# Kernel tuning notes

Measured on AMD Instinct MI355X. Metric: run time of the kernel, lower is better.

## Reference

```python
import jax, jax.numpy as jnp
import numpy as np

B, N = 128, 128
FEAT_IN = 6   # feature_dim(4) + class + score
E = 32        # embedding_dim
NUM_CLASSES = 80


def setup_inputs() -> dict:
    key = jax.random.key(0)
    ks = jax.random.split(key, 20)
    def glorot(k, shape):
        fan_in, fan_out = shape[0], shape[1]
        lim = jnp.sqrt(6.0 / (fan_in + fan_out)).astype(jnp.float32)
        return jax.random.uniform(k, shape, jnp.float32, -lim, lim)
    return {
        'boxes': jax.random.uniform(ks[0], (B, N, 4), jnp.float32),
        'classes': jax.random.randint(ks[1], (B, N), 0, NUM_CLASSES),
        'scores': jax.random.uniform(ks[2], (B, N), jnp.float32),
        'num_objects': jax.random.randint(ks[3], (B,), 1, N + 1),
        # feature_encoder: Linear(6->32), ReLU, Linear(32->32)
        'W1': glorot(ks[4], (FEAT_IN, E)), 'b1': jnp.zeros((E,), jnp.float32),
        'W2': glorot(ks[5], (E, E)),       'b2': jnp.zeros((E,), jnp.float32),
        # isObject: Linear(32->32), ReLU, Linear(32->1), Sigmoid
        'Wo1': glorot(ks[6], (E, E)),  'bo1': jnp.zeros((E,), jnp.float32),
        'Wo2': glorot(ks[7], (E, 1)),  'bo2': jnp.zeros((1,), jnp.float32),
        # sameClass: Linear(64->32), ReLU, Linear(32->1), Sigmoid
        'Ws1': glorot(ks[8], (2 * E, E)), 'bs1': jnp.zeros((E,), jnp.float32),
        'Ws2': glorot(ks[9], (E, 1)),     'bs2': jnp.zeros((1,), jnp.float32),
    }


def reference(boxes, classes, scores, num_objects, W1, b1, W2, b2,
              Wo1, bo1, Wo2, bo2, Ws1, bs1, Ws2, bs2):
    # encode: [B,N,6] -> [B,N,E]
    combined = jnp.concatenate(
        [boxes, classes.astype(jnp.float32)[..., None], scores[..., None]], axis=-1)
    enc = jax.nn.relu(combined @ W1 + b1) @ W2 + b2                 # [B,N,E]

    # isObject predicate -> [B,N]
    isobj = jax.nn.sigmoid(jax.nn.relu(enc @ Wo1 + bo1) @ Wo2 + bo2)[..., 0]

    # sameClass on all pairs: split concat-weight so we never build [B,N,N,2E]
    Wsx, Wsy = Ws1[:E], Ws1[E:]
    hx = enc @ Wsx                                                  # [B,N,E]
    hy = enc @ Wsy                                                  # [B,N,E]
    h = jax.nn.relu(hx[:, :, None, :] + hy[:, None, :, :] + bs1)    # [B,N,N,E]
    same = jax.nn.sigmoid(h @ Ws2 + bs2)[..., 0]                    # [B,N,N] (x,y)

    # inner = And_min(isObject(y), sameClass(x,y))
    inner = jnp.minimum(isobj[:, None, :], same)                    # [B,N,N]

    mask = jnp.arange(N)[None, :] < num_objects[:, None]            # [B,N] valid objs
    n = num_objects.astype(jnp.float32)
    denom = jnp.maximum(n, 1.0)

    # Exists_y = mean over valid y
    exists = jnp.sum(inner * mask[:, None, :], axis=-1) / denom[:, None]  # [B,N]

    # outer = Or_max(Not(isObject(x)), exists)
    outer = jnp.maximum(1.0 - isobj, exists)                        # [B,N]

    # Forall_x = min over valid x (pad with 1.0, never the min for valid batches)
    sat_b = jnp.min(jnp.where(mask, outer, 1.0), axis=-1)           # [B]

    valid = (num_objects > 0).astype(jnp.float32)
    cnt = jnp.sum(valid)
    total = jnp.where(cnt > 0,
                      jnp.sum(sat_b * valid) / jnp.maximum(cnt, 1.0),
                      jnp.float32(1.0))
    return total
```

## Files before the change

### kernel.cpp

```cpp
#include <hip/hip_runtime.h>

#define BB 128
#define NN 128
#define EE 32


__global__ __launch_bounds__(512) void ltn_fused(
    const float* __restrict__ boxes, const int* __restrict__ classes,
    const float* __restrict__ scores, const int* __restrict__ num_objects,
    const float* __restrict__ W1, const float* __restrict__ b1,
    const float* __restrict__ W2, const float* __restrict__ b2,
    const float* __restrict__ Wo1, const float* __restrict__ bo1,
    const float* __restrict__ Wo2, const float* __restrict__ bo2,
    const float* __restrict__ Ws1, const float* __restrict__ bs1,
    const float* __restrict__ Ws2, const float* __restrict__ bs2,
    float* __restrict__ ws)
{
    __shared__ float hyS[128 * 36];
    __shared__ float hxS[64 * 36];
    __shared__ float rows[32 * 36];
    __shared__ float isoS[128];
    __shared__ float wred[8];

    const int t = threadIdx.x;
    const int b = blockIdx.x >> 1;
    const int half = blockIdx.x & 1;
    const int e = t & 31;
    const int g = t >> 5;

    const int nb = num_objects[b];

    float w1c[6];
#pragma unroll
    for (int f = 0; f < 6; f++) w1c[f] = W1[f * 32 + e];
    float w2c[32], wo1c[32], wsxc[32], wsyc[32];
#pragma unroll
    for (int k = 0; k < 32; k++) {
        w2c[k]  = W2[k * 32 + e];
        wo1c[k] = Wo1[k * 32 + e];
        wsxc[k] = Ws1[k * 32 + e];
        wsyc[k] = Ws1[(32 + k) * 32 + e];
    }
    const float b1e  = b1[e];
    const float b2e  = b2[e];
    const float bo1e = bo1[e];
    const float wo2e = Wo2[e];
    const float bo2s = bo2[0];

    const int il0 = g * 8;
#pragma unroll 2
    for (int it = 0; it < 8; ++it) {
        const int il = il0 + it;
        const int item = b * 128 + il;
        float* row = rows + (g * 2 + (it & 1)) * 36;

        const float4 bx = ((const float4*)boxes)[item];
        const float c4 = (float)classes[item];
        const float c5 = scores[item];

        float h1 = b1e;
        h1 = fmaf(bx.x, w1c[0], h1);
        h1 = fmaf(bx.y, w1c[1], h1);
        h1 = fmaf(bx.z, w1c[2], h1);
        h1 = fmaf(bx.w, w1c[3], h1);
        h1 = fmaf(c4,   w1c[4], h1);
        h1 = fmaf(c5,   w1c[5], h1);
        h1 = fmaxf(h1, 0.f);

        row[e] = h1;

        float a0 = 0.f, a1 = 0.f, a2 = 0.f, a3 = 0.f;
#pragma unroll
        for (int kk = 0; kk < 8; kk++) {
            const float4 h = *(const float4*)(row + kk * 4);
            a0 = fmaf(h.x, w2c[4 * kk + 0], a0);
            a1 = fmaf(h.y, w2c[4 * kk + 1], a1);
            a2 = fmaf(h.z, w2c[4 * kk + 2], a2);
            a3 = fmaf(h.w, w2c[4 * kk + 3], a3);
        }
        const float enc = ((a0 + a1) + (a2 + a3)) + b2e;
        row[e] = enc;

        float u = bo1e, hx = 0.f, hy = 0.f;
#pragma unroll
        for (int kk = 0; kk < 8; kk++) {
            const float4 ec = *(const float4*)(row + kk * 4);
            const int k0 = 4 * kk;
            u  = fmaf(ec.x, wo1c[k0 + 0], u);
            u  = fmaf(ec.y, wo1c[k0 + 1], u);
            u  = fmaf(ec.z, wo1c[k0 + 2], u);
            u  = fmaf(ec.w, wo1c[k0 + 3], u);
            hx = fmaf(ec.x, wsxc[k0 + 0], hx);
            hx = fmaf(ec.y, wsxc[k0 + 1], hx);
            hx = fmaf(ec.z, wsxc[k0 + 2], hx);
            hx = fmaf(ec.w, wsxc[k0 + 3], hx);
            hy = fmaf(ec.x, wsyc[k0 + 0], hy);
            hy = fmaf(ec.y, wsyc[k0 + 1], hy);
            hy = fmaf(ec.z, wsyc[k0 + 2], hy);
            hy = fmaf(ec.w, wsyc[k0 + 3], hy);
        }
        u = fmaxf(u, 0.f);

        float v = u * wo2e;
        v += __shfl_xor(v, 16, 32);
        v += __shfl_xor(v, 8, 32);
        v += __shfl_xor(v, 4, 32);
        v += __shfl_xor(v, 2, 32);
        v += __shfl_xor(v, 1, 32);

        hyS[il * 36 + e] = hy;
        if ((il >> 6) == half) hxS[(il & 63) * 36 + e] = hx;
        if (e == 0)
            isoS[il] = 1.f / (1.f + __expf(-(v + bo2s)));
    }
    __syncthreads();

    const int p  = t >> 4;
    const int li0 = half * 64 + 2 * p;
    const int li1 = li0 + 1;
    const int s  = t & 15;

    float hxb0[32], hxb1[32];
#pragma unroll
    for (int kk = 0; kk < 8; kk++) {
        const float4 a = ((const float4*)(hxS + (2 * p) * 36))[kk];
        const float4 c = ((const float4*)(hxS + (2 * p + 1) * 36))[kk];
        const int k0 = 4 * kk;
        hxb0[k0 + 0] = a.x + bs1[k0 + 0];  hxb1[k0 + 0] = c.x + bs1[k0 + 0];
        hxb0[k0 + 1] = a.y + bs1[k0 + 1];  hxb1[k0 + 1] = c.y + bs1[k0 + 1];
        hxb0[k0 + 2] = a.z + bs1[k0 + 2];  hxb1[k0 + 2] = c.z + bs1[k0 + 2];
        hxb0[k0 + 3] = a.w + bs1[k0 + 3];  hxb1[k0 + 3] = c.w + bs1[k0 + 3];
    }
    float w2[32];
#pragma unroll
    for (int k = 0; k < 32; k++) w2[k] = Ws2[k];
    const float bbias = bs2[0];

    float acc0 = 0.f, acc1 = 0.f;
    for (int j = s; j < nb; j += 16) {
        const float4* hr4 = (const float4*)(hyS + j * 36);
        float d0 = bbias, d1 = 0.f, d2 = 0.f, d3 = 0.f;
        float e0 = bbias, e1 = 0.f, e2 = 0.f, e3 = 0.f;
#pragma unroll
        for (int kk = 0; kk < 8; kk++) {
            const float4 h = hr4[kk];
            const int k0 = 4 * kk;
            d0 = fmaf(fmaxf(hxb0[k0 + 0] + h.x, 0.f), w2[k0 + 0], d0);
            d1 = fmaf(fmaxf(hxb0[k0 + 1] + h.y, 0.f), w2[k0 + 1], d1);
            d2 = fmaf(fmaxf(hxb0[k0 + 2] + h.z, 0.f), w2[k0 + 2], d2);
            d3 = fmaf(fmaxf(hxb0[k0 + 3] + h.w, 0.f), w2[k0 + 3], d3);
            e0 = fmaf(fmaxf(hxb1[k0 + 0] + h.x, 0.f), w2[k0 + 0], e0);
            e1 = fmaf(fmaxf(hxb1[k0 + 1] + h.y, 0.f), w2[k0 + 1], e1);
            e2 = fmaf(fmaxf(hxb1[k0 + 2] + h.z, 0.f), w2[k0 + 2], e2);
            e3 = fmaf(fmaxf(hxb1[k0 + 3] + h.w, 0.f), w2[k0 + 3], e3);
        }
        const float dd = (d0 + d1) + (d2 + d3);
        const float ee = (e0 + e1) + (e2 + e3);
        const float same0 = 1.f / (1.f + __expf(-dd));
        const float same1 = 1.f / (1.f + __expf(-ee));
        const float iso_j = isoS[j];
        acc0 += fminf(iso_j, same0);
        acc1 += fminf(iso_j, same1);
    }
    acc0 += __shfl_xor(acc0, 1);  acc1 += __shfl_xor(acc1, 1);
    acc0 += __shfl_xor(acc0, 2);  acc1 += __shfl_xor(acc1, 2);
    acc0 += __shfl_xor(acc0, 4);  acc1 += __shfl_xor(acc1, 4);
    acc0 += __shfl_xor(acc0, 8);  acc1 += __shfl_xor(acc1, 8);

    const float denom = (float)(nb > 1 ? nb : 1);
    const float ex0 = acc0 / denom;
    const float ex1 = acc1 / denom;
    const float o0 = fmaxf(1.f - isoS[li0], ex0);
    const float o1 = fmaxf(1.f - isoS[li1], ex1);
    float val = fminf((li0 < nb) ? o0 : 1.f, (li1 < nb) ? o1 : 1.f);

    val = fminf(val, __shfl_xor(val, 16));
    val = fminf(val, __shfl_xor(val, 32));
    if ((t & 63) == 0) wred[t >> 6] = val;
    __syncthreads();

    if (t == 0) {
        float m = wred[0];
#pragma unroll
        for (int w = 1; w < 8; w++) m = fminf(m, wred[w]);
        ws[blockIdx.x] = m;
    }
}

__global__ __launch_bounds__(128) void finalize_kernel(
    const int* __restrict__ num_objects, const float* __restrict__ ws,
    float* __restrict__ out)
{
    __shared__ float r1[2], r2[2];
    const int t = threadIdx.x;
    const float sat = fminf(ws[2 * t], ws[2 * t + 1]);
    const float valid = (num_objects[t] > 0) ? 1.f : 0.f;
    float contrib = sat * valid;
    float vcnt = valid;
#pragma unroll
    for (int off = 1; off < 64; off <<= 1) {
        contrib += __shfl_xor(contrib, off);
        vcnt    += __shfl_xor(vcnt, off);
    }
    if ((t & 63) == 0) { r1[t >> 6] = contrib; r2[t >> 6] = vcnt; }
    __syncthreads();
    if (t == 0) {
        const float sc = r1[0] + r1[1];
        const float cn = r2[0] + r2[1];
        out[0] = (cn > 0.f) ? (sc / cn) : 1.f;
    }
}

extern "C" void kernel_launch(void* const* d_in, const int* in_sizes, int n_in,
                              void* d_out, int out_size, void* d_ws, size_t ws_size,
                              hipStream_t stream)
{
    const float* boxes       = (const float*)d_in[0];
    const int*   classes     = (const int*)d_in[1];
    const float* scores      = (const float*)d_in[2];
    const int*   num_objects = (const int*)d_in[3];
    const float* W1  = (const float*)d_in[4];
    const float* b1  = (const float*)d_in[5];
    const float* W2  = (const float*)d_in[6];
    const float* b2  = (const float*)d_in[7];
    const float* Wo1 = (const float*)d_in[8];
    const float* bo1 = (const float*)d_in[9];
    const float* Wo2 = (const float*)d_in[10];
    const float* bo2 = (const float*)d_in[11];
    const float* Ws1 = (const float*)d_in[12];
    const float* bs1 = (const float*)d_in[13];
    const float* Ws2 = (const float*)d_in[14];
    const float* bs2 = (const float*)d_in[15];

    float* ws  = (float*)d_ws;
    float* out = (float*)d_out;

    ltn_fused<<<256, 512, 0, stream>>>(boxes, classes, scores, num_objects,
                                       W1, b1, W2, b2, Wo1, bo1, Wo2, bo2,
                                       Ws1, bs1, Ws2, bs2, ws);
    finalize_kernel<<<1, 128, 0, stream>>>(num_objects, ws, out);
}
```

Before: 99.08 us.

## Restructure encoder to per-object threads with warp-specialized projection stages

```diff
diff --git a/kernel.cpp b/kernel.cpp
--- a/kernel.cpp
+++ b/kernel.cpp
@@ -5,7 +5,7 @@
 #define EE 32
 
 
-__global__ __launch_bounds__(512) void ltn_fused(
+__global__ __launch_bounds__(512, 2) void ltn_fused(
     const float* __restrict__ boxes, const int* __restrict__ classes,
     const float* __restrict__ scores, const int* __restrict__ num_objects,
     const float* __restrict__ W1, const float* __restrict__ b1,
@@ -16,102 +16,123 @@
     const float* __restrict__ Ws2, const float* __restrict__ bs2,
     float* __restrict__ ws)
 {
+    __shared__ float encS[128 * 36];
     __shared__ float hyS[128 * 36];
     __shared__ float hxS[64 * 36];
-    __shared__ float rows[32 * 36];
     __shared__ float isoS[128];
     __shared__ float wred[8];
 
     const int t = threadIdx.x;
     const int b = blockIdx.x >> 1;
     const int half = blockIdx.x & 1;
-    const int e = t & 31;
-    const int g = t >> 5;
+    const int w = t >> 6;
+    const int lane = t & 63;
 
     const int nb = num_objects[b];
 
-    float w1c[6];
-#pragma unroll
-    for (int f = 0; f < 6; f++) w1c[f] = W1[f * 32 + e];
-    float w2c[32], wo1c[32], wsxc[32], wsyc[32];
-#pragma unroll
-    for (int k = 0; k < 32; k++) {
-        w2c[k]  = W2[k * 32 + e];
-        wo1c[k] = Wo1[k * 32 + e];
-        wsxc[k] = Ws1[k * 32 + e];
-        wsyc[k] = Ws1[(32 + k) * 32 + e];
-    }
-    const float b1e  = b1[e];
-    const float b2e  = b2[e];
-    const float bo1e = bo1[e];
-    const float wo2e = Wo2[e];
-    const float bo2s = bo2[0];
-
-    const int il0 = g * 8;
-#pragma unroll 2
-    for (int it = 0; it < 8; ++it) {
-        const int il = il0 + it;
-        const int item = b * 128 + il;
-        float* row = rows + (g * 2 + (it & 1)) * 36;
-
+    if (w < 2) {
+        const int li = w * 64 + lane;
+        const int item = b * 128 + li;
         const float4 bx = ((const float4*)boxes)[item];
         const float c4 = (float)classes[item];
         const float c5 = scores[item];
 
-        float h1 = b1e;
-        h1 = fmaf(bx.x, w1c[0], h1);
-        h1 = fmaf(bx.y, w1c[1], h1);
-        h1 = fmaf(bx.z, w1c[2], h1);
-        h1 = fmaf(bx.w, w1c[3], h1);
-        h1 = fmaf(c4,   w1c[4], h1);
-        h1 = fmaf(c5,   w1c[5], h1);
-        h1 = fmaxf(h1, 0.f);
-
-        row[e] = h1;
-
-        float a0 = 0.f, a1 = 0.f, a2 = 0.f, a3 = 0.f;
+        float h1[32];
+#pragma unroll
+        for (int e = 0; e < 32; e++) {
+            float v = b1[e];
+            v = fmaf(bx.x, W1[0 * 32 + e], v);
+            v = fmaf(bx.y, W1[1 * 32 + e], v);
+            v = fmaf(bx.z, W1[2 * 32 + e], v);
+            v = fmaf(bx.w, W1[3 * 32 + e], v);
+            v = fmaf(c4,   W1[4 * 32 + e], v);
+            v = fmaf(c5,   W1[5 * 32 + e], v);
+            h1[e] = fmaxf(v, 0.f);
+        }
+        float enc[32];
+#pragma unroll
+        for (int e = 0; e < 32; e++) enc[e] = b2[e];
+#pragma unroll
+        for (int k = 0; k < 32; k++) {
+            const float hk = h1[k];
+#pragma unroll
+            for (int e = 0; e < 32; e++)
+                enc[e] = fmaf(hk, W2[k * 32 + e], enc[e]);
+        }
+        float* er = encS + li * 36;
+#pragma unroll
+        for (int kk = 0; kk < 8; kk++)
+            ((float4*)er)[kk] = make_float4(enc[4 * kk], enc[4 * kk + 1],
+                                            enc[4 * kk + 2], enc[4 * kk + 3]);
+    }
+    __syncthreads();
+
+    if (w >= 2 && w <= 5) {
+        const int hs = w & 1;
+        const int li = hs * 64 + lane;
+        float encR[32];
+        const float4* er4 = (const float4*)(encS + li * 36);
 #pragma unroll
         for (int kk = 0; kk < 8; kk++) {
-            const float4 h = *(const float4*)(row + kk * 4);
-            a0 = fmaf(h.x, w2c[4 * kk + 0], a0);
-            a1 = fmaf(h.y, w2c[4 * kk + 1], a1);
-            a2 = fmaf(h.z, w2c[4 * kk + 2], a2);
-            a3 = fmaf(h.w, w2c[4 * kk + 3], a3);
-        }
-        const float enc = ((a0 + a1) + (a2 + a3)) + b2e;
-        row[e] = enc;
-
-        float u = bo1e, hx = 0.f, hy = 0.f;
+            const float4 v = er4[kk];
+            encR[4 * kk] = v.x; encR[4 * kk + 1] = v.y;
+            encR[4 * kk + 2] = v.z; encR[4 * kk + 3] = v.w;
+        }
+        const float* M = (w <= 3) ? Wo1 : (Ws1 + 32 * 32);
+        float acc[32];
+        if (w <= 3) {
+#pragma unroll
+            for (int e = 0; e < 32; e++) acc[e] = bo1[e];
+        } else {
+#pragma unroll
+            for (int e = 0; e < 32; e++) acc[e] = 0.f;
+        }
+#pragma unroll
+        for (int k = 0; k < 32; k++) {
+            const float ek = encR[k];
+#pragma unroll
+            for (int e = 0; e < 32; e++)
+                acc[e] = fmaf(ek, M[k * 32 + e], acc[e]);
+        }
+        if (w <= 3) {
+            float z = bo2[0];
+#pragma unroll
+            for (int e = 0; e < 32; e++)
+                z = fmaf(fmaxf(acc[e], 0.f), Wo2[e], z);
+            isoS[li] = 1.f / (1.f + __expf(-z));
+        } else {
+            float* r = hyS + li * 36;
+#pragma unroll
+            for (int kk = 0; kk < 8; kk++)
+                ((float4*)r)[kk] = make_float4(acc[4 * kk], acc[4 * kk + 1],
+                                               acc[4 * kk + 2], acc[4 * kk + 3]);
+        }
+    } else if (w >= 6) {
+        const int li = half * 64 + lane;
+        const int eo = (w == 6) ? 0 : 16;
+        float encR[32];
+        const float4* er4 = (const float4*)(encS + li * 36);
 #pragma unroll
         for (int kk = 0; kk < 8; kk++) {
-            const float4 ec = *(const float4*)(row + kk * 4);
-            const int k0 = 4 * kk;
-            u  = fmaf(ec.x, wo1c[k0 + 0], u);
-            u  = fmaf(ec.y, wo1c[k0 + 1], u);
-            u  = fmaf(ec.z, wo1c[k0 + 2], u);
-            u  = fmaf(ec.w, wo1c[k0 + 3], u);
-            hx = fmaf(ec.x, wsxc[k0 + 0], hx);
-            hx = fmaf(ec.y, wsxc[k0 + 1], hx);
-            hx = fmaf(ec.z, wsxc[k0 + 2], hx);
-            hx = fmaf(ec.w, wsxc[k0 + 3], hx);
-            hy = fmaf(ec.x, wsyc[k0 + 0], hy);
-            hy = fmaf(ec.y, wsyc[k0 + 1], hy);
-            hy = fmaf(ec.z, wsyc[k0 + 2], hy);
-            hy = fmaf(ec.w, wsyc[k0 + 3], hy);
-        }
-        u = fmaxf(u, 0.f);
-
-        float v = u * wo2e;
-        v += __shfl_xor(v, 16, 32);
-        v += __shfl_xor(v, 8, 32);
-        v += __shfl_xor(v, 4, 32);
-        v += __shfl_xor(v, 2, 32);
-        v += __shfl_xor(v, 1, 32);
-
-        hyS[il * 36 + e] = hy;
-        if ((il >> 6) == half) hxS[(il & 63) * 36 + e] = hx;
-        if (e == 0)
-            isoS[il] = 1.f / (1.f + __expf(-(v + bo2s)));
+            const float4 v = er4[kk];
+            encR[4 * kk] = v.x; encR[4 * kk + 1] = v.y;
+            encR[4 * kk + 2] = v.z; encR[4 * kk + 3] = v.w;
+        }
+        float acc[16];
+#pragma unroll
+        for (int e = 0; e < 16; e++) acc[e] = 0.f;
+#pragma unroll
+        for (int k = 0; k < 32; k++) {
+            const float ek = encR[k];
+#pragma unroll
+            for (int e = 0; e < 16; e++)
+                acc[e] = fmaf(ek, Ws1[k * 32 + eo + e], acc[e]);
+        }
+        float* r = hxS + lane * 36 + eo;
+#pragma unroll
+        for (int kk = 0; kk < 4; kk++)
+            ((float4*)r)[kk] = make_float4(acc[4 * kk], acc[4 * kk + 1],
+                                           acc[4 * kk + 2], acc[4 * kk + 3]);
     }
     __syncthreads();
 
@@ -182,7 +203,7 @@
     if (t == 0) {
         float m = wred[0];
 #pragma unroll
-        for (int w = 1; w < 8; w++) m = fminf(m, wred[w]);
+        for (int ww = 1; ww < 8; ww++) m = fminf(m, wred[ww]);
         ws[blockIdx.x] = m;
     }
 }
```

Result: slower. 113.9 us (+15.0%).
